# Optimization experiments

Hardware: AMD Instinct MI355X
Metric: run time of the kernel (lower is better)

The kernel has to match this reference:

```python
import jax, jax.numpy as jnp
import numpy as np

B, N, L, K = 32, 512, 8, 8


def setup_inputs() -> dict:
    key = jax.random.key(0)
    k1, k2 = jax.random.split(key)
    A = jax.random.normal(k1, (B, N, N), dtype=jnp.float32)
    A = 0.5 * (A + A.transpose(0, 2, 1))  # symmetric matrix, as in MMF use-case
    O_stack = jax.random.normal(k2, (L, B, K, K), dtype=jnp.float32)  # per-level KxK rotations
    rng = np.random.default_rng(0)
    idx = np.stack([np.sort(rng.choice(N, K, replace=False)) for _ in range(B * L)])
    indices = jnp.asarray(idx.reshape(B, L, K), dtype=jnp.int32)  # sorted, distinct per (b,l)
    wavelet = indices[:, :, 0]  # wavelet index is one of the selected indices per level
    return {"A": A, "O_stack": O_stack, "indices": indices, "wavelet": wavelet}


def reference(A, O_stack, indices, wavelet):
    Bz, Nz, _ = A.shape
    Lz = O_stack.shape[0]
    eye = jnp.eye(Nz, dtype=A.dtype)

    def build_U(idx, O):
        # identity except the KxK block at (idx_i, idx_j) replaced by O
        # (matches torch boolean-mask row-major fill since idx is sorted)
        return eye.at[idx[:, None], idx[None, :]].set(O)

    right = None
    for l in range(Lz):
        U = jax.vmap(build_U)(indices[:, l], O_stack[l])  # [B,N,N]
        right = U if l == 0 else U @ right
        A = U @ A @ U.transpose(0, 2, 1)

    # final masking: zero rows/cols of wavelet indices, keep diagonal
    active = jnp.ones((Bz, Nz), dtype=A.dtype).at[jnp.arange(Bz)[:, None], wavelet].set(0.0)
    left = active[:, :, None] * active[:, None, :]
    d = jnp.arange(Nz)
    left = left.at[:, d, d].set(1.0)
    D = A * left
    A_rec = right.transpose(0, 2, 1) @ D @ right
    return (A_rec, right, D)
```

## Files before the change

### kernel.cpp

```cpp
#include <hip/hip_runtime.h>

#define BATCH 32
#define NDIM 512
#define LNUM 8
#define KDIM 8

#define WS_PM     0
#define WS_S      512
#define WS_ACT    640
#define WS_W      1152
#define WS_B2     5248
#define WS_C2     9344
#define WS_RA     13440
#define WS_RD     46208
#define WS_RAT    78976
#define WS_RDT    111744
#define WS_STRIDE 144512

#define LSTR 65
typedef float f4 __attribute__((ext_vector_type(4)));

__global__ __launch_bounds__(256) void k_prep(
    const float* __restrict__ A, const float* __restrict__ O,
    const int* __restrict__ indices, const int* __restrict__ wavelet,
    float* __restrict__ ws)
{
    const int b  = blockIdx.x;
    const int cy = blockIdx.y;
    const int tid = threadIdx.x;
    float* base = ws + (size_t)b * WS_STRIDE;

    __shared__ float Wl[64*LSTR];
    __shared__ float Buf1[64*LSTR];
    __shared__ float Buf2[64*LSTR];
    __shared__ float Buf3[64*LSTR];
    __shared__ int   pml[NDIM];
    __shared__ float actl[NDIM];
    __shared__ float actS[64];
    __shared__ int   idxsh[64];
    __shared__ int   Ssh[64];
    __shared__ int   prow[KDIM];
    __shared__ float Oall[LNUM*KDIM*KDIM];
    __shared__ int   s_sh;

    for (int t = tid; t < LNUM*KDIM*KDIM; t += 256) {
        int l = t >> 6, k = t & 63;
        Oall[t] = O[((size_t)l*BATCH + b)*(KDIM*KDIM) + k];
    }
    if (tid < 64) idxsh[tid] = indices[b*64 + tid];
    for (int n = tid; n < NDIM; n += 256) { pml[n] = -1; actl[n] = 1.f; }
    __syncthreads();

    if (tid < 64) {
        int n = idxsh[tid];
        bool first = true;
        for (int t = 0; t < tid; ++t) if (idxsh[t] == n) first = false;
        unsigned long long m = __ballot(first);
        int rank = __popcll(m & ((1ull << tid) - 1ull));
        if (first) { pml[n] = rank; Ssh[rank] = n; }
        if (tid == 0) s_sh = (int)__popcll(m);
    }
    if (tid >= 64 && tid < 64 + LNUM) {
        actl[wavelet[b*LNUM + (tid - 64)]] = 0.f;
    }
    __syncthreads();
    const int s = s_sh;
    if (tid < 64 && tid >= s) Ssh[tid] = 0;
    __syncthreads();
    if (tid < 64) actS[tid] = actl[Ssh[tid]];

    for (int t = tid; t < 4096; t += 256) {
        int rr = t >> 6, cc = t & 63;
        Wl[rr*LSTR + cc] = (rr == cc && rr < s) ? 1.f : 0.f;
    }
    __syncthreads();
    for (int l = 0; l < LNUM; ++l) {
        if (tid < KDIM) prow[tid] = pml[idxsh[l*KDIM + tid]];
        __syncthreads();
        for (int t = tid; t < KDIM*64; t += 256) {
            int i = t >> 6, c = t & 63;
            float acc = 0.f;
            #pragma unroll
            for (int j = 0; j < KDIM; ++j)
                acc += Oall[l*64 + i*KDIM + j] * Wl[prow[j]*LSTR + c];
            Buf3[t] = acc;
        }
        __syncthreads();
        for (int t = tid; t < KDIM*64; t += 256) {
            int i = t >> 6, c = t & 63;
            Wl[prow[i]*LSTR + c] = Buf3[t];
        }
        __syncthreads();
    }

    if (cy < 8) {
        const int j0 = cy * 64;
        float* AS  = Buf1;
        float* RAt = Buf2;
        float* g_RA  = base + WS_RA;
        float* g_RD  = base + WS_RD;
        float* g_RAT = base + WS_RAT;
        float* g_RDT = base + WS_RDT;

        for (int t = tid; t < 1024; t += 256) {
            int n = t >> 4, cc = (t & 15) * 4;
            f4 v = ((const f4*)(A + ((size_t)b*NDIM + Ssh[n])*NDIM + j0))[t & 15];
            AS[n*64 + cc]   = v.x; AS[n*64 + cc+1] = v.y;
            AS[n*64 + cc+2] = v.z; AS[n*64 + cc+3] = v.w;
        }
        __syncthreads();

        const int g = tid >> 6;
        const int j = tid & 63;
        float racc[16];

        #pragma unroll
        for (int k = 0; k < 16; ++k) racc[k] = 0.f;
        for (int n = 0; n < 64; ++n) {
            float av = AS[n*64 + j];
            #pragma unroll
            for (int k = 0; k < 16; ++k) racc[k] += Wl[(g*16 + k)*LSTR + n] * av;
        }
        #pragma unroll
        for (int k = 0; k < 16; ++k) {
            RAt[(g*16 + k)*64 + j] = racc[k];
            g_RA[(g*16 + k)*NDIM + j0 + j] = racc[k];
        }
        {
            f4* dst = (f4*)(g_RAT + (size_t)(j0 + j)*64 + g*16);
            #pragma unroll
            for (int q = 0; q < 4; ++q) {
                f4 v = { racc[4*q], racc[4*q+1], racc[4*q+2], racc[4*q+3] };
                dst[q] = v;
            }
        }
        __syncthreads();

        #pragma unroll
        for (int k = 0; k < 16; ++k) racc[k] = 0.f;
        for (int n = 0; n < 64; ++n) {
            float dt = actS[n] * RAt[n*64 + j];
            #pragma unroll
            for (int k = 0; k < 16; ++k) racc[k] += Wl[n*LSTR + g*16 + k] * dt;
        }
        const float aj = actl[j0 + j];
        #pragma unroll
        for (int k = 0; k < 16; ++k) {
            float rd = racc[k] * aj;
            racc[k] = rd;
            g_RD[(g*16 + k)*NDIM + j0 + j] = rd;
        }
        {
            f4* dst = (f4*)(g_RDT + (size_t)(j0 + j)*64 + g*16);
            #pragma unroll
            for (int q = 0; q < 4; ++q) {
                f4 v = { racc[4*q], racc[4*q+1], racc[4*q+2], racc[4*q+3] };
                dst[q] = v;
            }
        }
    } else {
        {
            int*   g_posmap = (int*)(base + WS_PM);
            float* g_act    = base + WS_ACT;
            float* g_W      = base + WS_W;
            for (int n = tid; n < NDIM; n += 256) { g_posmap[n] = pml[n]; g_act[n] = actl[n]; }
            for (int t = tid; t < 4096; t += 256) g_W[t] = Wl[(t>>6)*LSTR + (t&63)];
        }

        for (int t = tid; t < 4096; t += 256) {
            int n = t >> 6, m = t & 63;
            Buf1[n*LSTR + m] = A[((size_t)b*NDIM + Ssh[n])*NDIM + Ssh[m]];
        }
        __syncthreads();

        const int w = tid >> 6;
        const int ln = tid & 63;
        float acc[16];

        #pragma unroll
        for (int k = 0; k < 16; ++k) acc[k] = 0.f;
        for (int n = 0; n < 64; ++n) {
            float as = Buf1[n*LSTR + ln];
            #pragma unroll
            for (int k = 0; k < 16; ++k) acc[k] += Wl[(w*16 + k)*LSTR + n] * as;
        }
        #pragma unroll
        for (int k = 0; k < 16; ++k) Buf2[(w*16 + k)*LSTR + ln] = acc[k];
        __syncthreads();

        #pragma unroll
        for (int k = 0; k < 16; ++k) acc[k] = 0.f;
        for (int m = 0; m < 64; ++m) {
            float wv = Wl[ln*LSTR + m];
            #pragma unroll
            for (int k = 0; k < 16; ++k) acc[k] += Buf2[(w*16 + k)*LSTR + m] * wv;
        }
        #pragma unroll
        for (int k = 0; k < 16; ++k) Buf3[(w*16 + k)*LSTR + ln] = acc[k];
        __syncthreads();
        {
            float* g_B2 = base + WS_B2;
            for (int t = tid; t < 4096; t += 256) g_B2[t] = Buf3[(t>>6)*LSTR + (t&63)];
        }

        for (int t = tid; t < 4096; t += 256) {
            int n = t >> 6, m = t & 63;
            float mv = (Ssh[n] == Ssh[m]) ? 1.f : actS[n]*actS[m];
            Buf1[n*LSTR + m] = mv * Buf3[n*LSTR + m];
        }
        __syncthreads();

        #pragma unroll
        for (int k = 0; k < 16; ++k) acc[k] = 0.f;
        for (int n = 0; n < 64; ++n) {
            float dv = Buf1[n*LSTR + ln];
            #pragma unroll
            for (int k = 0; k < 16; ++k) acc[k] += Wl[n*LSTR + (w*16 + k)] * dv;
        }
        #pragma unroll
        for (int k = 0; k < 16; ++k) Buf2[(w*16 + k)*LSTR + ln] = acc[k];
        __syncthreads();

        #pragma unroll
        for (int k = 0; k < 16; ++k) acc[k] = 0.f;
        for (int m = 0; m < 64; ++m) {
            float wv = Wl[m*LSTR + ln];
            #pragma unroll
            for (int k = 0; k < 16; ++k) acc[k] += Buf2[(w*16 + k)*LSTR + m] * wv;
        }
        {
            float* g_C2 = base + WS_C2;
            #pragma unroll
            for (int k = 0; k < 16; ++k) g_C2[(w*16 + k)*64 + ln] = acc[k];
        }
    }
}

__global__ __launch_bounds__(256) void k_big(const float* __restrict__ A,
                                             const float* __restrict__ ws,
                                             float* __restrict__ out)
{
    const int b = blockIdx.y;
    const int rh = threadIdx.x >> 7;
    const int lane = threadIdx.x & 127;
    const int i = blockIdx.x*2 + rh;
    const int j0 = lane*4;

    const float* base = ws + (size_t)b * WS_STRIDE;
    const int*   posmap = (const int*)(base + WS_PM);
    const float* act = base + WS_ACT;
    const float* g_W  = base + WS_W;
    const float* g_B2 = base + WS_B2;
    const float* g_C2 = base + WS_C2;
    const float* RA  = base + WS_RA;
    const float* RD  = base + WS_RD;
    const float* RAT = base + WS_RAT;
    const float* RDT = base + WS_RDT;

    const int pi = posmap[i];
    const float acti = act[i];
    const size_t rowoff = ((size_t)b*NDIM + i)*NDIM;
    const size_t seg = (size_t)BATCH*NDIM*NDIM;

    int4   p4  = ((const int4*)posmap)[lane];
    float4 aj4 = ((const float4*)act)[lane];
    int   pm[4] = {p4.x, p4.y, p4.z, p4.w};
    float aj[4] = {aj4.x, aj4.y, aj4.z, aj4.w};

    float a[4], arec[4], dv[4], rv[4];

    if (pi < 0) {
        const float* rat = RAT + (size_t)i*64;
        const float* rdt = RDT + (size_t)i*64;
        f4 v = __builtin_nontemporal_load((const f4*)(A + rowoff) + lane);
        a[0]=v.x; a[1]=v.y; a[2]=v.z; a[3]=v.w;
        #pragma unroll
        for (int c = 0; c < 4; ++c) {
            int pj = pm[c];
            if (pj >= 0) a[c] = rat[pj];
            float mv = (i == j0 + c) ? 1.f : acti * aj[c];
            dv[c] = a[c] * mv;
            arec[c] = (pj < 0) ? dv[c] : rdt[pj];
            rv[c] = (i == j0 + c) ? 1.f : 0.f;
        }
    } else {
        f4 v = ((const f4*)(RA + (size_t)pi*NDIM))[lane];
        f4 w = ((const f4*)(RD + (size_t)pi*NDIM))[lane];
        a[0]=v.x; a[1]=v.y; a[2]=v.z; a[3]=v.w;
        arec[0]=w.x; arec[1]=w.y; arec[2]=w.z; arec[3]=w.w;
        #pragma unroll
        for (int c = 0; c < 4; ++c) {
            int pj = pm[c];
            if (pj >= 0) {
                a[c]    = g_B2[pi*64 + pj];
                arec[c] = g_C2[pi*64 + pj];
                rv[c]   = g_W[pi*64 + pj];
            } else {
                rv[c] = 0.f;
            }
            float mv = (i == j0 + c) ? 1.f : acti * aj[c];
            dv[c] = a[c] * mv;
        }
    }

    f4 o0; o0.x = arec[0]; o0.y = arec[1]; o0.z = arec[2]; o0.w = arec[3];
    f4 o1; o1.x = rv[0];   o1.y = rv[1];   o1.z = rv[2];   o1.w = rv[3];
    f4 o2; o2.x = dv[0];   o2.y = dv[1];   o2.z = dv[2];   o2.w = dv[3];
    __builtin_nontemporal_store(o0, (f4*)(out + rowoff) + lane);
    __builtin_nontemporal_store(o1, (f4*)(out + seg + rowoff) + lane);
    __builtin_nontemporal_store(o2, (f4*)(out + 2*seg + rowoff) + lane);
}

extern "C" void kernel_launch(void* const* d_in, const int* in_sizes, int n_in,
                              void* d_out, int out_size, void* d_ws, size_t ws_size,
                              hipStream_t stream) {
    const float* A       = (const float*)d_in[0];
    const float* O       = (const float*)d_in[1];
    const int*   indices = (const int*)d_in[2];
    const int*   wavelet = (const int*)d_in[3];
    float* ws  = (float*)d_ws;
    float* out = (float*)d_out;

    k_prep<<<dim3(BATCH, 9), 256, 0, stream>>>(A, O, indices, wavelet, ws);
    k_big <<<dim3(NDIM/2, BATCH), 256, 0, stream>>>(A, ws, out);
}
```

Baseline: 178.6 us.

## Overlap W composition on one wavefront with A gathers on the other three

Builds the 64x64 rotation composition W entirely inside wavefront 0, with each lane owning one column. This removes the many block-wide barriers per level. Meanwhile the other three wavefronts gather rows of A into shared memory and write posmap and activity vectors, so the prep latency overlaps with global loads. It also uses vectorized float4 shared stores for the row tile. The risk is that the serial per-lane W update on a single wavefront becomes the critical path if the loads finish first.

```diff
diff --git a/kernel.cpp b/kernel.cpp
--- a/kernel.cpp
+++ b/kernel.cpp
@@ -31,17 +31,15 @@
     float* base = ws + (size_t)b * WS_STRIDE;
 
     __shared__ float Wl[64*LSTR];
-    __shared__ float Buf1[64*LSTR];
-    __shared__ float Buf2[64*LSTR];
-    __shared__ float Buf3[64*LSTR];
+    __shared__ __align__(16) float Buf1[64*LSTR];
+    __shared__ __align__(16) float Buf2[64*LSTR];
+    __shared__ __align__(16) float Buf3[64*LSTR];
     __shared__ int   pml[NDIM];
     __shared__ float actl[NDIM];
     __shared__ float actS[64];
     __shared__ int   idxsh[64];
     __shared__ int   Ssh[64];
-    __shared__ int   prow[KDIM];
     __shared__ float Oall[LNUM*KDIM*KDIM];
-    __shared__ int   s_sh;
 
     for (int t = tid; t < LNUM*KDIM*KDIM; t += 256) {
         int l = t >> 6, k = t & 63;
@@ -51,47 +49,66 @@
     for (int n = tid; n < NDIM; n += 256) { pml[n] = -1; actl[n] = 1.f; }
     __syncthreads();
 
-    if (tid < 64) {
-        int n = idxsh[tid];
+    const int wv = tid >> 6;
+    const int ln = tid & 63;
+    int s_reg = 0;
+
+    if (wv == 0) {
+        int n = idxsh[ln];
         bool first = true;
-        for (int t = 0; t < tid; ++t) if (idxsh[t] == n) first = false;
+        for (int t = 0; t < ln; ++t) if (idxsh[t] == n) first = false;
         unsigned long long m = __ballot(first);
-        int rank = __popcll(m & ((1ull << tid) - 1ull));
+        int rank = __popcll(m & ((1ull << ln) - 1ull));
+        s_reg = (int)__popcll(m);
         if (first) { pml[n] = rank; Ssh[rank] = n; }
-        if (tid == 0) s_sh = (int)__popcll(m);
-    }
-    if (tid >= 64 && tid < 64 + LNUM) {
-        actl[wavelet[b*LNUM + (tid - 64)]] = 0.f;
+        if (ln >= s_reg) Ssh[ln] = 0;
+        if (ln < LNUM) actl[wavelet[b*LNUM + ln]] = 0.f;
     }
     __syncthreads();
-    const int s = s_sh;
-    if (tid < 64 && tid >= s) Ssh[tid] = 0;
+
+    if (wv == 0) {
+        actS[ln] = actl[Ssh[ln]];
+        for (int rr = 0; rr < 64; ++rr)
+            Wl[rr*LSTR + ln] = (rr == ln && rr < s_reg) ? 1.f : 0.f;
+        for (int l = 0; l < LNUM; ++l) {
+            int pr[KDIM];
+            float wcol[KDIM], accv[KDIM];
+            #pragma unroll
+            for (int j = 0; j < KDIM; ++j) pr[j] = pml[idxsh[l*KDIM + j]];
+            #pragma unroll
+            for (int j = 0; j < KDIM; ++j) wcol[j] = Wl[pr[j]*LSTR + ln];
+            #pragma unroll
+            for (int i = 0; i < KDIM; ++i) {
+                float a = 0.f;
+                #pragma unroll
+                for (int j = 0; j < KDIM; ++j)
+                    a += Oall[l*64 + i*KDIM + j] * wcol[j];
+                accv[i] = a;
+            }
+            #pragma unroll
+            for (int i = 0; i < KDIM; ++i) Wl[pr[i]*LSTR + ln] = accv[i];
+        }
+    } else {
+        if (cy < 8) {
+            const int j0 = cy * 64;
+            for (int t = tid - 64; t < 1024; t += 192) {
+                int n = t >> 4, cc = t & 15;
+                f4 v = ((const f4*)(A + ((size_t)b*NDIM + Ssh[n])*NDIM + j0))[cc];
+                ((f4*)(Buf1 + n*64))[cc] = v;
+            }
+        } else {
+            for (int t = tid - 64; t < 4096; t += 192) {
+                int n = t >> 6, mm = t & 63;
+                Buf1[n*LSTR + mm] = A[((size_t)b*NDIM + Ssh[n])*NDIM + Ssh[mm]];
+            }
+            int*   g_posmap = (int*)(base + WS_PM);
+            float* g_act    = base + WS_ACT;
+            for (int n = tid - 64; n < NDIM; n += 192) {
+                g_posmap[n] = pml[n]; g_act[n] = actl[n];
+            }
+        }
+    }
     __syncthreads();
-    if (tid < 64) actS[tid] = actl[Ssh[tid]];
-
-    for (int t = tid; t < 4096; t += 256) {
-        int rr = t >> 6, cc = t & 63;
-        Wl[rr*LSTR + cc] = (rr == cc && rr < s) ? 1.f : 0.f;
-    }
-    __syncthreads();
-    for (int l = 0; l < LNUM; ++l) {
-        if (tid < KDIM) prow[tid] = pml[idxsh[l*KDIM + tid]];
-        __syncthreads();
-        for (int t = tid; t < KDIM*64; t += 256) {
-            int i = t >> 6, c = t & 63;
-            float acc = 0.f;
-            #pragma unroll
-            for (int j = 0; j < KDIM; ++j)
-                acc += Oall[l*64 + i*KDIM + j] * Wl[prow[j]*LSTR + c];
-            Buf3[t] = acc;
-        }
-        __syncthreads();
-        for (int t = tid; t < KDIM*64; t += 256) {
-            int i = t >> 6, c = t & 63;
-            Wl[prow[i]*LSTR + c] = Buf3[t];
-        }
-        __syncthreads();
-    }
 
     if (cy < 8) {
         const int j0 = cy * 64;
@@ -102,16 +119,8 @@
         float* g_RAT = base + WS_RAT;
         float* g_RDT = base + WS_RDT;
 
-        for (int t = tid; t < 1024; t += 256) {
-            int n = t >> 4, cc = (t & 15) * 4;
-            f4 v = ((const f4*)(A + ((size_t)b*NDIM + Ssh[n])*NDIM + j0))[t & 15];
-            AS[n*64 + cc]   = v.x; AS[n*64 + cc+1] = v.y;
-            AS[n*64 + cc+2] = v.z; AS[n*64 + cc+3] = v.w;
-        }
-        __syncthreads();
-
-        const int g = tid >> 6;
-        const int j = tid & 63;
+        const int g = wv;
+        const int j = ln;
         float racc[16];
 
         #pragma unroll
@@ -160,21 +169,11 @@
         }
     } else {
         {
-            int*   g_posmap = (int*)(base + WS_PM);
-            float* g_act    = base + WS_ACT;
-            float* g_W      = base + WS_W;
-            for (int n = tid; n < NDIM; n += 256) { g_posmap[n] = pml[n]; g_act[n] = actl[n]; }
+            float* g_W = base + WS_W;
             for (int t = tid; t < 4096; t += 256) g_W[t] = Wl[(t>>6)*LSTR + (t&63)];
         }
 
-        for (int t = tid; t < 4096; t += 256) {
-            int n = t >> 6, m = t & 63;
-            Buf1[n*LSTR + m] = A[((size_t)b*NDIM + Ssh[n])*NDIM + Ssh[m]];
-        }
-        __syncthreads();
-
-        const int w = tid >> 6;
-        const int ln = tid & 63;
+        const int w = wv;
         float acc[16];
 
         #pragma unroll
@@ -191,9 +190,9 @@
         #pragma unroll
         for (int k = 0; k < 16; ++k) acc[k] = 0.f;
         for (int m = 0; m < 64; ++m) {
-            float wv = Wl[ln*LSTR + m];
-            #pragma unroll
-            for (int k = 0; k < 16; ++k) acc[k] += Buf2[(w*16 + k)*LSTR + m] * wv;
+            float wvv = Wl[ln*LSTR + m];
+            #pragma unroll
+            for (int k = 0; k < 16; ++k) acc[k] += Buf2[(w*16 + k)*LSTR + m] * wvv;
         }
         #pragma unroll
         for (int k = 0; k < 16; ++k) Buf3[(w*16 + k)*LSTR + ln] = acc[k];
@@ -224,9 +223,9 @@
         #pragma unroll
         for (int k = 0; k < 16; ++k) acc[k] = 0.f;
         for (int m = 0; m < 64; ++m) {
-            float wv = Wl[m*LSTR + ln];
-            #pragma unroll
-            for (int k = 0; k < 16; ++k) acc[k] += Buf2[(w*16 + k)*LSTR + m] * wv;
+            float wvv = Wl[m*LSTR + ln];
+            #pragma unroll
+            for (int k = 0; k < 16; ++k) acc[k] += Buf2[(w*16 + k)*LSTR + m] * wvv;
         }
         {
             float* g_C2 = base + WS_C2;
```

Measured after the change: 175.8 us. Within noise of the previous version (-1.6%).
